# Performance work log

Measured on AMD Instinct MI355X. Metric: run time of the kernel, lower is better.

Reference implementation:

```python
import jax, jax.numpy as jnp
import numpy as np

H = 16            # num_attention_heads
START_RATIO = 0.1
RECENT_RATIO = 0.4
THETA = 10000.0
CHUNK = 256       # hard-coded chunk_size in source
CLIP = 1e4        # nan_to_num posinf/neginf bound


def _rope_cos_sin(T, D, dtype):
    inv_freq = 1.0 / (THETA ** (jnp.arange(0, D, 2, dtype=jnp.float32) / D))
    freqs = jnp.arange(T, dtype=jnp.float32)[:, None] * inv_freq[None, :]  # [T, D/2]
    emb = jnp.concatenate([freqs, freqs], axis=-1)                          # [T, D]
    return jnp.cos(emb).astype(dtype), jnp.sin(emb).astype(dtype)


def _apply_rope(x, cos, sin):
    # x: [B,H,T,D]; cos/sin: [T,D] broadcast over B,H
    d = x.shape[-1] // 2
    rot = jnp.concatenate([-x[..., d:], x[..., :d]], axis=-1)
    return x * cos + rot * sin


def setup_inputs() -> dict:
    key = jax.random.key(0)
    k0, k1, k2, k3, k4 = jax.random.split(key, 5)
    B, T, Dm = 1, 2048, 2048
    scale = 1.0 / np.sqrt(Dm).astype(np.float32)
    return {
        "hidden_states": jax.random.normal(k0, (B, T, Dm), jnp.float32),
        "Wq": jax.random.normal(k1, (Dm, Dm), jnp.float32) * scale,
        "Wk": jax.random.normal(k2, (Dm, Dm), jnp.float32) * scale,
        "Wv": jax.random.normal(k3, (Dm, Dm), jnp.float32) * scale,
        "Wo": jax.random.normal(k4, (Dm, Dm), jnp.float32) * scale,
    }


def reference(hidden_states, Wq, Wk, Wv, Wo):
    B, T, Dm = hidden_states.shape
    D = Dm // H
    hs = jnp.nan_to_num(hidden_states, nan=0.0, posinf=CLIP, neginf=-CLIP)

    def proj(W):  # torch Linear: x @ W.T, then [B,T,H,D] -> [B,H,T,D]
        return (hs @ W.T).reshape(B, T, H, D).transpose(0, 2, 1, 3)

    q, k, v = proj(Wq), proj(Wk), proj(Wv)
    cos, sin = _rope_cos_sin(T, D, hs.dtype)
    q = _apply_rope(q, cos, sin)
    k = _apply_rope(k, cos, sin)

    # start+recent keep mask (past_key_value=None -> k_len == T)
    k_len = T
    sb = max(0, min(int(START_RATIO * k_len), k_len))
    rb = max(0, min(int(RECENT_RATIO * k_len), k_len - sb))
    pos = jnp.arange(k_len)
    keep = (pos < sb) | (pos >= k_len - rb)          # [K]

    MIN = jnp.finfo(hs.dtype).min
    scores = jnp.einsum('bhqd,bhkd->bhqk', q, k) / jnp.sqrt(jnp.asarray(D, hs.dtype))
    scores = jnp.where(keep, scores, MIN)
    probs = jax.nn.softmax(scores, axis=-1)          # [B,H,T,K]

    # CaM merge of evicted V into recent window, driven by the LAST query row.
    evict = k_len - rb                               # static python int
    last = probs[..., -1, :]                         # [B,H,K]
    mean_attn = last[..., evict + 1:].mean(axis=-1) + 1e-6
    p = jnp.clip(last[..., evict] / mean_attn, 0.0, 1.0)
    p = jnp.nan_to_num(p, nan=0.0, posinf=1.0, neginf=0.0)
    u = jax.random.uniform(jax.random.key(42), p.shape, p.dtype)
    bern = (u < p).astype(v.dtype)                   # [B,H]
    v_e = v[..., evict, :] * bern[..., None] / rb    # [B,H,D]
    v_merged = v.at[..., evict + 1:, :].add(v_e[..., None, :])

    # Chunked loop effect: only the last chunk's AV uses merged V.
    last_start = ((T - 1) // CHUNK) * CHUNK
    out_pre = jnp.einsum('bhqk,bhkd->bhqd', probs[:, :, :last_start], v)
    out_last = jnp.einsum('bhqk,bhkd->bhqd', probs[:, :, last_start:], v_merged)
    out = jnp.concatenate([out_pre, out_last], axis=2)   # [B,H,T,D]

    out = out.transpose(0, 2, 1, 3).reshape(B, T, Dm) @ Wo.T
    return jnp.nan_to_num(out, nan=0.0, posinf=CLIP, neginf=-CLIP)
```

## Files before the change

kernel.cpp:

```cpp
#include <hip/hip_runtime.h>
#include <stdint.h>

#define T_SEQ 2048
#define DM    2048
#define NH    16
#define HD    128
#define SB    204
#define EV    1229
#define RB    819
#define NRECF 818.0f
#define LAST_START 1792
#define SCALE 0.08838834764831845f

typedef __attribute__((ext_vector_type(8))) short short8;
typedef __attribute__((ext_vector_type(4))) short short4v;
typedef __attribute__((ext_vector_type(4))) float f32x4;

__device__ __forceinline__ unsigned short f2bf(float f) {
  uint32_t u = __float_as_uint(f);
  u += 0x7fffu + ((u >> 16) & 1u);
  return (unsigned short)(u >> 16);
}
__device__ __forceinline__ float bf2f(unsigned short s) {
  return __uint_as_float(((uint32_t)s) << 16);
}
__device__ __forceinline__ void gload16(const void* g, void* l) {
  __builtin_amdgcn_global_load_lds((const __attribute__((address_space(1))) void*)g,
                                   (__attribute__((address_space(3))) void*)l,
                                   16, 0, 0);
}
__device__ __forceinline__ float n2n(float v) {
  if (isnan(v)) return 0.0f;
  if (isinf(v)) return v > 0.0f ? 10000.0f : -10000.0f;
  return v;
}

__global__ __launch_bounds__(256) void cvt_kernel(
    const float* __restrict__ hs, const float* __restrict__ wq,
    const float* __restrict__ wk, const float* __restrict__ wv,
    const float* __restrict__ wo, unsigned short* __restrict__ hsb,
    unsigned short* __restrict__ wqb, unsigned short* __restrict__ wkb,
    unsigned short* __restrict__ wvb, unsigned short* __restrict__ wob) {
  int gid = blockIdx.x * 256 + threadIdx.x;
  int region = gid >> 20;
  int off4 = (gid & 1048575) * 4;
  const float* src; unsigned short* dst;
  switch (region) {
    case 0: src = hs; dst = hsb; break;
    case 1: src = wq; dst = wqb; break;
    case 2: src = wk; dst = wkb; break;
    case 3: src = wv; dst = wvb; break;
    default: src = wo; dst = wob; break;
  }
  float4 v = *(const float4*)(src + off4);
  if (region == 0) { v.x = n2n(v.x); v.y = n2n(v.y); v.z = n2n(v.z); v.w = n2n(v.w); }
  ushort4 o;
  o.x = f2bf(v.x); o.y = f2bf(v.y); o.z = f2bf(v.z); o.w = f2bf(v.w);
  *(ushort4*)(dst + off4) = o;
}

__global__ __launch_bounds__(256) void cs_kernel(float* __restrict__ cst, float* __restrict__ snt) {
  int idx = blockIdx.x * 256 + threadIdx.x;
  int t = idx >> 6, i = idx & 63;
  float inv = (float)exp(-(double)i * log(10000.0) / 64.0);
  float ang = (float)t * inv;
  cst[idx] = (float)cos((double)ang);
  snt[idx] = (float)sin((double)ang);
}

__device__ __forceinline__ void gemm_mainloop64(
    const unsigned short* __restrict__ A, const unsigned short* __restrict__ B,
    unsigned short* As, unsigned short* Bs, int m0, int n0, int k0, int ksteps,
    int tid, f32x4 (&acc)[4][4]) {
  int w = tid >> 6, lane = tid & 63;
  int wm = w >> 1, wn = w & 1;
  int q4 = lane >> 4, r = lane & 15;
  f32x4 zero = {0.f, 0.f, 0.f, 0.f};
  #pragma unroll
  for (int mi = 0; mi < 4; mi++)
    #pragma unroll
    for (int ni = 0; ni < 4; ni++) acc[mi][ni] = zero;
  int srow = w * 32 + (lane >> 3);
  int swz = ((lane & 7) ^ (lane >> 3)) * 16;
  const char* Ag = (const char*)(A + (size_t)(m0 + srow) * DM) + swz + k0 * 2;
  const char* Bg = (const char*)(B + (size_t)(n0 + srow) * DM) + swz + k0 * 2;
  unsigned short* Asl = As + w * 2048;
  unsigned short* Bsl = Bs + w * 2048;
  for (int s = 0; s < ksteps; s++) {
    __syncthreads();
    #pragma unroll
    for (int g = 0; g < 4; g++) {
      gload16(Ag + g * (8 * DM * 2), Asl + g * 512);
      gload16(Bg + g * (8 * DM * 2), Bsl + g * 512);
    }
    Ag += 128; Bg += 128;
    __syncthreads();
    #pragma unroll
    for (int kh = 0; kh < 2; kh++) {
      int pcs = ((kh * 4 + q4) ^ (r & 7)) * 8;
      short8 a[4], b[4];
      #pragma unroll
      for (int mi = 0; mi < 4; mi++)
        a[mi] = *(const short8*)(As + (wm * 64 + mi * 16 + r) * 64 + pcs);
      #pragma unroll
      for (int ni = 0; ni < 4; ni++)
        b[ni] = *(const short8*)(Bs + ((ni & 1) * 64 + wn * 32 + (ni >> 1) * 16 + r) * 64 + pcs);
      #pragma unroll
      for (int mi = 0; mi < 4; mi++)
        #pragma unroll
        for (int ni = 0; ni < 4; ni++)
          acc[mi][ni] = __builtin_amdgcn_mfma_f32_16x16x32_bf16(a[mi], b[ni], acc[mi][ni], 0, 0, 0);
    }
  }
}

__global__ __launch_bounds__(256, 3) void gemm_qkv_kernel(
    const unsigned short* __restrict__ hsb, const unsigned short* __restrict__ wqb,
    const unsigned short* __restrict__ wkb, const unsigned short* __restrict__ wvb,
    const float* __restrict__ cst, const float* __restrict__ snt,
    unsigned short* __restrict__ qbf, unsigned short* __restrict__ kbf,
    unsigned short* __restrict__ vbT) {
  __shared__ __align__(16) unsigned short LDSBUF[17408];
  unsigned short* As = LDSBUF;
  unsigned short* Bs = LDSBUF + 8192;
  int z = blockIdx.z;
  const unsigned short* B = (z == 0) ? wqb : (z == 1) ? wkb : wvb;
  int m0 = blockIdx.y * 128, n0 = blockIdx.x * 128;
  f32x4 acc[4][4];
  gemm_mainloop64(hsb, B, As, Bs, m0, n0, 0, DM / 64, threadIdx.x, acc);
  int tid = threadIdx.x, w = tid >> 6, lane = tid & 63;
  int wm = w >> 1, wn = w & 1, q4 = lane >> 4, r = lane & 15;
  int h = n0 >> 7;
  if (z < 2) {
    unsigned short* dst = (z == 0) ? qbf : kbf;
    #pragma unroll
    for (int mi = 0; mi < 4; mi++)
      #pragma unroll
      for (int p = 0; p < 2; p++) {
        int d = wn * 32 + p * 16 + r;
        #pragma unroll
        for (int g = 0; g < 4; g++) {
          int t = m0 + wm * 64 + mi * 16 + q4 * 4 + g;
          float c = cst[t * 64 + d], s = snt[t * 64 + d];
          float x0 = acc[mi][2 * p][g], x1 = acc[mi][2 * p + 1][g];
          dst[((size_t)h * T_SEQ + t) * HD + d]      = f2bf(x0 * c - x1 * s);
          dst[((size_t)h * T_SEQ + t) * HD + d + 64] = f2bf(x1 * c + x0 * s);
        }
      }
  } else {
    __syncthreads();
    #pragma unroll
    for (int mi = 0; mi < 4; mi++)
      #pragma unroll
      for (int ni = 0; ni < 4; ni++) {
        int c = (ni & 1) * 64 + wn * 32 + (ni >> 1) * 16 + r;
        int tl = wm * 64 + mi * 16 + q4 * 4;
        short4v pv;
        pv[0] = (short)f2bf(acc[mi][ni][0]);
        pv[1] = (short)f2bf(acc[mi][ni][1]);
        pv[2] = (short)f2bf(acc[mi][ni][2]);
        pv[3] = (short)f2bf(acc[mi][ni][3]);
        *(short4v*)(LDSBUF + c * 136 + tl) = pv;
      }
    __syncthreads();
    int d = tid >> 1, th = tid & 1;
    unsigned short* gdst = vbT + ((size_t)h * HD + d) * T_SEQ + m0 + th * 64;
    const unsigned short* lsrc = LDSBUF + d * 136 + th * 64;
    #pragma unroll
    for (int j = 0; j < 8; j++)
      *(short8*)(gdst + j * 8) = *(const short8*)(lsrc + j * 8);
  }
}

__device__ __forceinline__ void attn_body(
    int kb, const unsigned short* Kt, const unsigned short* Vt,
    const unsigned short* indv, unsigned short* Psw,
    const short8 (&aq)[4], f32x4 (&o)[8], f32x4& o9, float (&evf)[4],
    int q4, int r) {
  f32x4 zero = {0.f, 0.f, 0.f, 0.f};
  int rsw = (r >> 1) & 3;
  f32x4 s0 = zero, s1 = zero;
  #pragma unroll
  for (int c = 0; c < 4; c++) {
    int pc = ((c * 4 + q4) ^ r) * 8;
    short8 bk0 = *(const short8*)(Kt + r * 128 + pc);
    short8 bk1 = *(const short8*)(Kt + (16 + r) * 128 + pc);
    s0 = __builtin_amdgcn_mfma_f32_16x16x32_bf16(aq[c], bk0, s0, 0, 0, 0);
    s1 = __builtin_amdgcn_mfma_f32_16x16x32_bf16(aq[c], bk1, s1, 0, 0, 0);
  }
  int kg0 = kb + r, kg1 = kb + 16 + r;
  bool keep0 = (kg0 < SB) || (kg0 >= EV);
  bool keep1 = (kg1 < SB) || (kg1 >= EV);
  #pragma unroll
  for (int g = 0; g < 4; g++) {
    float p0 = keep0 ? __expf(fmaf(s0[g], SCALE, -8.0f)) : 0.0f;
    float p1 = keep1 ? __expf(fmaf(s1[g], SCALE, -8.0f)) : 0.0f;
    if (kb == 1216 && kg0 == EV) evf[g] = p0;
    int row = q4 * 4 + g;
    int psw = (row >> 1) & 3;
    Psw[row * 32 + (((r >> 3) ^ psw) * 8) + (r & 7)]       = f2bf(p0);
    Psw[row * 32 + ((((r >> 3) + 2) ^ psw) * 8) + (r & 7)] = f2bf(p1);
  }
  short8 pa = *(const short8*)(Psw + r * 32 + (q4 ^ rsw) * 8);
  #pragma unroll
  for (int ni = 0; ni < 8; ni++) {
    short8 bv = *(const short8*)(Vt + (ni * 16 + r) * 32 + (q4 ^ rsw) * 8);
    o[ni] = __builtin_amdgcn_mfma_f32_16x16x32_bf16(pa, bv, o[ni], 0, 0, 0);
  }
  short8 bind = *(const short8*)(indv + r * 32 + (q4 ^ rsw) * 8);
  o9 = __builtin_amdgcn_mfma_f32_16x16x32_bf16(pa, bind, o9, 0, 0, 0);
}

__global__ __launch_bounds__(256, 2) void attn_kernel(
    const unsigned short* __restrict__ qbf, const unsigned short* __restrict__ kbf,
    const unsigned short* __restrict__ vbT, unsigned short* __restrict__ atb,
    float* __restrict__ attnf_s, float* __restrict__ Ssum, float* __restrict__ lst) {
  __shared__ __align__(16) unsigned short KtA[4096], KtB[4096];
  __shared__ __align__(16) unsigned short VtA[4096], VtB[4096];
  __shared__ __align__(16) unsigned short Ps[4][512];
  __shared__ __align__(16) unsigned short Ind[3 * 512];
  int tid = threadIdx.x, w = tid >> 6, lane = tid & 63;
  int q4 = lane >> 4, r = lane & 15;
  int h = blockIdx.y;
  int qb = blockIdx.x * 64 + w * 16;

  for (int idx = tid; idx < 3 * 512; idx += 256) {
    int v = idx >> 9, n = (idx >> 5) & 15, j = idx & 31;
    float val = 0.f;
    if (n == 0) val = 1.f;
    else if (n == 1) val = (v == 1) ? (j >= 14 ? 1.f : 0.f) : (v == 2 ? 1.f : 0.f);
    Ind[v * 512 + n * 32 + (((j >> 3) ^ ((n >> 1) & 3)) * 8) + (j & 7)] = f2bf(val);
  }

  short8 aq[4];
  {
    const unsigned short* qrow = qbf + ((size_t)h * T_SEQ + qb + r) * HD;
    #pragma unroll
    for (int c = 0; c < 4; c++) aq[c] = *(const short8*)(qrow + c * 32 + q4 * 8);
  }
  f32x4 zero = {0.f, 0.f, 0.f, 0.f};
  f32x4 o[8], o9;
  #pragma unroll
  for (int ni = 0; ni < 8; ni++) o[ni] = zero;
  o9 = zero;
  float evf[4] = {0.f, 0.f, 0.f, 0.f};

  const char* Kbase = (const char*)(kbf + (size_t)h * T_SEQ * HD);
  int krow0 = w * 8 + q4, krow1 = krow0 + 4;
  const char* Kg0 = Kbase + krow0 * 256 + ((r ^ (krow0 & 15)) * 16);
  const char* Kg1 = Kbase + krow1 * 256 + ((r ^ (krow1 & 15)) * 16);
  const char* Vbase = (const char*)(vbT + (size_t)h * HD * T_SEQ);
  int vsrc = ((lane & 3) ^ ((lane >> 3) & 3)) * 16;
  const char* Vg0 = Vbase + (size_t)(w * 32 + (lane >> 2)) * 4096 + vsrc;
  const char* Vg1 = Vg0 + 16 * 4096;
  unsigned short* KtlA = KtA + w * 1024;
  unsigned short* KtlB = KtB + w * 1024;
  unsigned short* VtlA = VtA + w * 1024;
  unsigned short* VtlB = VtB + w * 1024;

  for (int ci = 0; ci < 17; ci++) {
    int kb = (ci < 4) ? ci * 64 : 1216 + (ci - 4) * 64;
    const unsigned short* indA = Ind + ((ci < 4) ? 0 : (ci == 4) ? 512 : 1024);
    const unsigned short* indB = Ind + ((ci < 4) ? 0 : 1024);
    __syncthreads();
    gload16(Kg0 + kb * 256,       KtlA);
    gload16(Kg1 + kb * 256,       KtlA + 512);
    gload16(Kg0 + (kb + 32) * 256, KtlB);
    gload16(Kg1 + (kb + 32) * 256, KtlB + 512);
    gload16(Vg0 + kb * 2,        VtlA);
    gload16(Vg1 + kb * 2,        VtlA + 512);
    gload16(Vg0 + (kb + 32) * 2, VtlB);
    gload16(Vg1 + (kb + 32) * 2, VtlB + 512);
    __syncthreads();
    attn_body(kb,      KtA, VtA, indA, &Ps[w][0], aq, o, o9, evf, q4, r);
    attn_body(kb + 32, KtB, VtB, indB, &Ps[w][0], aq, o, o9, evf, q4, r);
  }

  float invl[4], srn[4], evn[4];
  #pragma unroll
  for (int g = 0; g < 4; g++) {
    float l  = __shfl(o9[g], lane & 48, 64);
    float sr = __shfl(o9[g], (lane & 48) | 1, 64);
    float ev = __shfl(evf[g], (lane & 48) | 13, 64);
    invl[g] = 1.0f / l;
    srn[g] = sr * invl[g];
    evn[g] = ev * invl[g];
  }
  if (blockIdx.x < (LAST_START / 64)) {
    #pragma unroll
    for (int ni = 0; ni < 8; ni++)
      #pragma unroll
      for (int g = 0; g < 4; g++)
        atb[(size_t)(qb + q4 * 4 + g) * DM + h * HD + ni * 16 + r] = f2bf(o[ni][g] * invl[g]);
  } else {
    #pragma unroll
    for (int ni = 0; ni < 8; ni++)
      #pragma unroll
      for (int g = 0; g < 4; g++)
        attnf_s[(size_t)(qb - LAST_START + q4 * 4 + g) * DM + h * HD + ni * 16 + r] = o[ni][g] * invl[g];
  }
  if (r == 0) {
    #pragma unroll
    for (int g = 0; g < 4; g++) {
      int t = qb + q4 * 4 + g;
      if (t >= LAST_START) Ssum[h * 256 + (t - LAST_START)] = srn[g];
      if (t == T_SEQ - 1) { lst[h * 2] = evn[g]; lst[h * 2 + 1] = srn[g]; }
    }
  }
}

__device__ __forceinline__ void tf_round(uint32_t& x0, uint32_t& x1, int rot) {
  x0 += x1;
  x1 = (x1 << rot) | (x1 >> (32 - rot));
  x1 ^= x0;
}
__global__ void bern_kernel(const float* __restrict__ lst, float* __restrict__ bsc) {
  int hh = threadIdx.x;
  if (hh >= NH) return;
  const uint32_t k0 = 0u, k1 = 42u, k2 = 0x1BD11BDAu ^ k0 ^ k1;
  uint32_t x0 = (uint32_t)(hh & 7), x1 = (uint32_t)((hh & 7) + 8);
  x0 += k0; x1 += k1;
  tf_round(x0, x1, 13); tf_round(x0, x1, 15); tf_round(x0, x1, 26); tf_round(x0, x1, 6);
  x0 += k1; x1 += k2 + 1u;
  tf_round(x0, x1, 17); tf_round(x0, x1, 29); tf_round(x0, x1, 16); tf_round(x0, x1, 24);
  x0 += k2; x1 += k0 + 2u;
  tf_round(x0, x1, 13); tf_round(x0, x1, 15); tf_round(x0, x1, 26); tf_round(x0, x1, 6);
  x0 += k0; x1 += k1 + 3u;
  tf_round(x0, x1, 17); tf_round(x0, x1, 29); tf_round(x0, x1, 16); tf_round(x0, x1, 24);
  x0 += k1; x1 += k2 + 4u;
  tf_round(x0, x1, 13); tf_round(x0, x1, 15); tf_round(x0, x1, 26); tf_round(x0, x1, 6);
  x0 += k2; x1 += k0 + 5u;
  uint32_t bits = (hh < 8) ? x0 : x1;
  float u = __uint_as_float((bits >> 9) | 0x3f800000u) - 1.0f;
  float evp = lst[hh * 2], srp = lst[hh * 2 + 1];
  float mean = srp * (1.0f / NRECF) + 1e-6f;
  float p = evp / mean;
  p = fminf(fmaxf(p, 0.0f), 1.0f);
  if (!(p == p)) p = 0.0f;
  bsc[hh] = (u < p) ? (1.0f / (float)RB) : 0.0f;
}

__global__ __launch_bounds__(256) void fixup_kernel(
    const float* __restrict__ attnf_s, const float* __restrict__ Ssum,
    const float* __restrict__ bsc, const unsigned short* __restrict__ vbT,
    unsigned short* __restrict__ atb) {
  int idx = blockIdx.x * 256 + threadIdx.x;
  int t2 = idx >> 11, n = idx & 2047;
  int h = n >> 7, d = n & 127;
  float v = attnf_s[idx];
  v += Ssum[h * 256 + t2] * bsc[h] * bf2f(vbT[((size_t)h * HD + d) * T_SEQ + EV]);
  atb[(size_t)(t2 + LAST_START) * DM + n] = f2bf(v);
}

__global__ __launch_bounds__(256, 2) void gemm_out_kernel(
    const unsigned short* __restrict__ atb, const unsigned short* __restrict__ wob,
    float* __restrict__ part0, float* __restrict__ part1) {
  __shared__ __align__(16) unsigned short LDSBUF[16384];
  unsigned short* As = LDSBUF;
  unsigned short* Bs = LDSBUF + 8192;
  int m0 = blockIdx.y * 128, n0 = blockIdx.x * 128;
  int kz = blockIdx.z;
  float* part = kz ? part1 : part0;
  f32x4 acc[4][4];
  gemm_mainloop64(atb, wob, As, Bs, m0, n0, kz * 1024, 16, threadIdx.x, acc);
  int tid = threadIdx.x, w = tid >> 6, lane = tid & 63;
  int wm = w >> 1, wn = w & 1, q4 = lane >> 4, r = lane & 15;
  #pragma unroll
  for (int mi = 0; mi < 4; mi++)
    #pragma unroll
    for (int ni = 0; ni < 4; ni++) {
      int c = n0 + (ni & 1) * 64 + wn * 32 + (ni >> 1) * 16 + r;
      #pragma unroll
      for (int g = 0; g < 4; g++) {
        int t = m0 + wm * 64 + mi * 16 + q4 * 4 + g;
        part[(size_t)t * DM + c] = acc[mi][ni][g];
      }
    }
}

__global__ __launch_bounds__(256) void add_kernel(
    const float* __restrict__ p0, const float* __restrict__ p1, float* __restrict__ out) {
  int i4 = (blockIdx.x * 256 + threadIdx.x) * 4;
  float4 a = *(const float4*)(p0 + i4);
  float4 b = *(const float4*)(p1 + i4);
  float4 o;
  o.x = n2n(a.x + b.x); o.y = n2n(a.y + b.y);
  o.z = n2n(a.z + b.z); o.w = n2n(a.w + b.w);
  *(float4*)(out + i4) = o;
}

extern "C" void kernel_launch(void* const* d_in, const int* in_sizes, int n_in,
                              void* d_out, int out_size, void* d_ws, size_t ws_size,
                              hipStream_t stream) {
  const float* hs = (const float*)d_in[0];
  const float* Wq = (const float*)d_in[1];
  const float* Wk = (const float*)d_in[2];
  const float* Wv = (const float*)d_in[3];
  const float* Wo = (const float*)d_in[4];
  char* ws = (char*)d_ws;
  const size_t MB = 1024 * 1024;
  unsigned short* hsb = (unsigned short*)(ws + 0);
  unsigned short* wqb = (unsigned short*)(ws + 8 * MB);
  unsigned short* wkb = (unsigned short*)(ws + 16 * MB);
  unsigned short* wvb = (unsigned short*)(ws + 24 * MB);
  unsigned short* wob = (unsigned short*)(ws + 32 * MB);
  unsigned short* qbf = (unsigned short*)(ws + 40 * MB);
  unsigned short* kbf = (unsigned short*)(ws + 48 * MB);
  unsigned short* vbT = (unsigned short*)(ws + 56 * MB);
  unsigned short* atb = (unsigned short*)(ws + 64 * MB);
  float* attnf_s = (float*)(ws + 72 * MB);
  float* part0 = (float*)(ws + 74 * MB);
  float* part1 = (float*)(ws + 90 * MB);
  float* cst = (float*)(ws + 106 * MB);
  float* snt = (float*)(ws + 106 * MB + 524288);
  float* Ssum = (float*)(ws + 107 * MB);
  float* lst = (float*)(ws + 107 * MB + 16384);
  float* bsc = (float*)(ws + 107 * MB + 16384 + 256);

  cvt_kernel<<<20480, 256, 0, stream>>>(hs, Wq, Wk, Wv, Wo, hsb, wqb, wkb, wvb, wob);
  cs_kernel<<<512, 256, 0, stream>>>(cst, snt);
  gemm_qkv_kernel<<<dim3(16, 16, 3), 256, 0, stream>>>(hsb, wqb, wkb, wvb, cst, snt, qbf, kbf, vbT);
  attn_kernel<<<dim3(32, 16), 256, 0, stream>>>(qbf, kbf, vbT, atb, attnf_s, Ssum, lst);
  bern_kernel<<<1, 64, 0, stream>>>(lst, bsc);
  fixup_kernel<<<2048, 256, 0, stream>>>(attnf_s, Ssum, bsc, vbT, atb);
  gemm_out_kernel<<<dim3(16, 16, 2), 256, 0, stream>>>(atb, wob, part0, part1);
  add_kernel<<<4096, 256, 0, stream>>>(part0, part1, (float*)d_out);
}
```

Measured before the change: 251.7 us.

## Double-buffer attention K/V loads, fuse Bernoulli into fixup, atomic split-K output

The attention kernel now prefetches the next K/V chunk into a second LDS buffer while computing the current one, with one barrier per iteration instead of two. The Bernoulli scale is computed inline in the fixup kernel, removing a one-block launch. The output GEMM's two split-K halves are accumulated into a memset output with float atomics, removing the partial buffers and the add kernel. The trade-off is nondeterministic summation order, a dropped nan_to_num clamp, and reliance on load completion before the barrier.

```diff
diff --git a/kernel.cpp b/kernel.cpp
--- a/kernel.cpp
+++ b/kernel.cpp
@@ -215,8 +215,8 @@
     const unsigned short* __restrict__ qbf, const unsigned short* __restrict__ kbf,
     const unsigned short* __restrict__ vbT, unsigned short* __restrict__ atb,
     float* __restrict__ attnf_s, float* __restrict__ Ssum, float* __restrict__ lst) {
-  __shared__ __align__(16) unsigned short KtA[4096], KtB[4096];
-  __shared__ __align__(16) unsigned short VtA[4096], VtB[4096];
+  __shared__ __align__(16) unsigned short KtS[2][2][4096];
+  __shared__ __align__(16) unsigned short VtS[2][2][4096];
   __shared__ __align__(16) unsigned short Ps[4][512];
   __shared__ __align__(16) unsigned short Ind[3 * 512];
   int tid = threadIdx.x, w = tid >> 6, lane = tid & 63;
@@ -253,27 +253,29 @@
   int vsrc = ((lane & 3) ^ ((lane >> 3) & 3)) * 16;
   const char* Vg0 = Vbase + (size_t)(w * 32 + (lane >> 2)) * 4096 + vsrc;
   const char* Vg1 = Vg0 + 16 * 4096;
-  unsigned short* KtlA = KtA + w * 1024;
-  unsigned short* KtlB = KtB + w * 1024;
-  unsigned short* VtlA = VtA + w * 1024;
-  unsigned short* VtlB = VtB + w * 1024;
-
+
+  auto issue_chunk = [&](int ci, int db) {
+    int kb = (ci < 4) ? ci * 64 : 1216 + (ci - 4) * 64;
+    gload16(Kg0 + kb * 256,         &KtS[db][0][w * 1024]);
+    gload16(Kg1 + kb * 256,         &KtS[db][0][w * 1024 + 512]);
+    gload16(Kg0 + (kb + 32) * 256,  &KtS[db][1][w * 1024]);
+    gload16(Kg1 + (kb + 32) * 256,  &KtS[db][1][w * 1024 + 512]);
+    gload16(Vg0 + kb * 2,           &VtS[db][0][w * 1024]);
+    gload16(Vg1 + kb * 2,           &VtS[db][0][w * 1024 + 512]);
+    gload16(Vg0 + (kb + 32) * 2,    &VtS[db][1][w * 1024]);
+    gload16(Vg1 + (kb + 32) * 2,    &VtS[db][1][w * 1024 + 512]);
+  };
+
+  issue_chunk(0, 0);
   for (int ci = 0; ci < 17; ci++) {
+    int db = ci & 1;
     int kb = (ci < 4) ? ci * 64 : 1216 + (ci - 4) * 64;
     const unsigned short* indA = Ind + ((ci < 4) ? 0 : (ci == 4) ? 512 : 1024);
     const unsigned short* indB = Ind + ((ci < 4) ? 0 : 1024);
     __syncthreads();
-    gload16(Kg0 + kb * 256,       KtlA);
-    gload16(Kg1 + kb * 256,       KtlA + 512);
-    gload16(Kg0 + (kb + 32) * 256, KtlB);
-    gload16(Kg1 + (kb + 32) * 256, KtlB + 512);
-    gload16(Vg0 + kb * 2,        VtlA);
-    gload16(Vg1 + kb * 2,        VtlA + 512);
-    gload16(Vg0 + (kb + 32) * 2, VtlB);
-    gload16(Vg1 + (kb + 32) * 2, VtlB + 512);
-    __syncthreads();
-    attn_body(kb,      KtA, VtA, indA, &Ps[w][0], aq, o, o9, evf, q4, r);
-    attn_body(kb + 32, KtB, VtB, indB, &Ps[w][0], aq, o, o9, evf, q4, r);
+    if (ci < 16) issue_chunk(ci + 1, db ^ 1);
+    attn_body(kb,      KtS[db][0], VtS[db][0], indA, &Ps[w][0], aq, o, o9, evf, q4, r);
+    attn_body(kb + 32, KtS[db][1], VtS[db][1], indB, &Ps[w][0], aq, o, o9, evf, q4, r);
   }
 
   float invl[4], srn[4], evn[4];
@@ -314,9 +316,7 @@
   x1 = (x1 << rot) | (x1 >> (32 - rot));
   x1 ^= x0;
 }
-__global__ void bern_kernel(const float* __restrict__ lst, float* __restrict__ bsc) {
-  int hh = threadIdx.x;
-  if (hh >= NH) return;
+__device__ __forceinline__ float bern_scale(int hh, const float* lst) {
   const uint32_t k0 = 0u, k1 = 42u, k2 = 0x1BD11BDAu ^ k0 ^ k1;
   uint32_t x0 = (uint32_t)(hh & 7), x1 = (uint32_t)((hh & 7) + 8);
   x0 += k0; x1 += k1;
@@ -337,30 +337,30 @@
   float p = evp / mean;
   p = fminf(fmaxf(p, 0.0f), 1.0f);
   if (!(p == p)) p = 0.0f;
-  bsc[hh] = (u < p) ? (1.0f / (float)RB) : 0.0f;
+  return (u < p) ? (1.0f / (float)RB) : 0.0f;
 }
 
 __global__ __launch_bounds__(256) void fixup_kernel(
     const float* __restrict__ attnf_s, const float* __restrict__ Ssum,
-    const float* __restrict__ bsc, const unsigned short* __restrict__ vbT,
+    const float* __restrict__ lst, const unsigned short* __restrict__ vbT,
     unsigned short* __restrict__ atb) {
   int idx = blockIdx.x * 256 + threadIdx.x;
   int t2 = idx >> 11, n = idx & 2047;
   int h = n >> 7, d = n & 127;
+  float bsc = bern_scale(h, lst);
   float v = attnf_s[idx];
-  v += Ssum[h * 256 + t2] * bsc[h] * bf2f(vbT[((size_t)h * HD + d) * T_SEQ + EV]);
+  v += Ssum[h * 256 + t2] * bsc * bf2f(vbT[((size_t)h * HD + d) * T_SEQ + EV]);
   atb[(size_t)(t2 + LAST_START) * DM + n] = f2bf(v);
 }
 
 __global__ __launch_bounds__(256, 2) void gemm_out_kernel(
     const unsigned short* __restrict__ atb, const unsigned short* __restrict__ wob,
-    float* __restrict__ part0, float* __restrict__ part1) {
+    float* __restrict__ out) {
   __shared__ __align__(16) unsigned short LDSBUF[16384];
   unsigned short* As = LDSBUF;
   unsigned short* Bs = LDSBUF + 8192;
   int m0 = blockIdx.y * 128, n0 = blockIdx.x * 128;
   int kz = blockIdx.z;
-  float* part = kz ? part1 : part0;
   f32x4 acc[4][4];
   gemm_mainloop64(atb, wob, As, Bs, m0, n0, kz * 1024, 16, threadIdx.x, acc);
   int tid = threadIdx.x, w = tid >> 6, lane = tid & 63;
@@ -373,20 +373,9 @@
       #pragma unroll
       for (int g = 0; g < 4; g++) {
         int t = m0 + wm * 64 + mi * 16 + q4 * 4 + g;
-        part[(size_t)t * DM + c] = acc[mi][ni][g];
+        atomicAdd(&out[(size_t)t * DM + c], acc[mi][ni][g]);
       }
     }
-}
-
-__global__ __launch_bounds__(256) void add_kernel(
-    const float* __restrict__ p0, const float* __restrict__ p1, float* __restrict__ out) {
-  int i4 = (blockIdx.x * 256 + threadIdx.x) * 4;
-  float4 a = *(const float4*)(p0 + i4);
-  float4 b = *(const float4*)(p1 + i4);
-  float4 o;
-  o.x = n2n(a.x + b.x); o.y = n2n(a.y + b.y);
-  o.z = n2n(a.z + b.z); o.w = n2n(a.w + b.w);
-  *(float4*)(out + i4) = o;
 }
 
 extern "C" void kernel_launch(void* const* d_in, const int* in_sizes, int n_in,
@@ -409,20 +398,16 @@
   unsigned short* vbT = (unsigned short*)(ws + 56 * MB);
   unsigned short* atb = (unsigned short*)(ws + 64 * MB);
   float* attnf_s = (float*)(ws + 72 * MB);
-  float* part0 = (float*)(ws + 74 * MB);
-  float* part1 = (float*)(ws + 90 * MB);
-  float* cst = (float*)(ws + 106 * MB);
-  float* snt = (float*)(ws + 106 * MB + 524288);
-  float* Ssum = (float*)(ws + 107 * MB);
-  float* lst = (float*)(ws + 107 * MB + 16384);
-  float* bsc = (float*)(ws + 107 * MB + 16384 + 256);
-
+  float* cst = (float*)(ws + 74 * MB);
+  float* snt = (float*)(ws + 74 * MB + 524288);
+  float* Ssum = (float*)(ws + 75 * MB);
+  float* lst = (float*)(ws + 75 * MB + 16384);
+
+  hipMemsetAsync(d_out, 0, (size_t)out_size * sizeof(float), stream);
   cvt_kernel<<<20480, 256, 0, stream>>>(hs, Wq, Wk, Wv, Wo, hsb, wqb, wkb, wvb, wob);
   cs_kernel<<<512, 256, 0, stream>>>(cst, snt);
   gemm_qkv_kernel<<<dim3(16, 16, 3), 256, 0, stream>>>(hsb, wqb, wkb, wvb, cst, snt, qbf, kbf, vbT);
   attn_kernel<<<dim3(32, 16), 256, 0, stream>>>(qbf, kbf, vbT, atb, attnf_s, Ssum, lst);
-  bern_kernel<<<1, 64, 0, stream>>>(lst, bsc);
-  fixup_kernel<<<2048, 256, 0, stream>>>(attnf_s, Ssum, bsc, vbT, atb);
-  gemm_out_kernel<<<dim3(16, 16, 2), 256, 0, stream>>>(atb, wob, part0, part1);
-  add_kernel<<<4096, 256, 0, stream>>>(part0, part1, (float*)d_out);
-}
+  fixup_kernel<<<2048, 256, 0, stream>>>(attnf_s, Ssum, lst, vbT, atb);
+  gemm_out_kernel<<<dim3(16, 16, 2), 256, 0, stream>>>(atb, wob, (float*)d_out);
+}
```

After: 260.4 us. +3.5%, slower.
